# Kernel tuning notes

Hardware: AMD Instinct MI355X
Metric: run time of the kernel (lower is better)

## Reference

```python
import jax, jax.numpy as jnp
import numpy as np

B, S, F = 4, 2048, 256
H, D = 8, 32            # n_heads, width_embedding; H*D == F
LN_EPS = 1e-3           # tf.keras LayerNormalization default epsilon


def setup_inputs() -> dict:
    key = jax.random.key(0)
    ks = jax.random.split(key, 6)
    s = 1.0 / np.sqrt(F)
    return {
        "x": jax.random.normal(ks[0], (B, S, F), dtype=jnp.float32),
        "Wq": jax.random.normal(ks[1], (F, H * D), dtype=jnp.float32) * s,
        "Wk": jax.random.normal(ks[2], (F, H * D), dtype=jnp.float32) * s,
        "Wv": jax.random.normal(ks[3], (F, H * D), dtype=jnp.float32) * s,
        "Wf": jax.random.normal(ks[4], (H * D, F), dtype=jnp.float32) * s,
        "bf": jnp.zeros((F,), dtype=jnp.float32),
    }


def reference(x, Wq, Wk, Wv, Wf, bf):
    # QKV projections (no bias), split heads: [B,S,H*D] -> [B,H,S,D]
    def split(t):
        return t.reshape(B, S, H, D).transpose(0, 2, 1, 3)

    q = split(x @ Wq) / jnp.sqrt(jnp.asarray(H, x.dtype))  # NOTE: module scales by sqrt(n_heads)
    k = split(x @ Wk)
    v = split(x @ Wv)

    scores = jnp.einsum("bhsd,bhtd->bhst", q, k)          # [B,H,S,S]
    attn = jax.nn.softmax(scores, axis=-1)
    ctx = jnp.einsum("bhst,bhtd->bhsd", attn, v)           # [B,H,S,D]

    y = ctx.transpose(0, 2, 1, 3).reshape(B, S, H * D)     # merge heads
    y = jax.nn.relu(y @ Wf + bf)                            # final dense with relu

    # residual + LayerNorm(center=False, scale=False)
    z = x + y
    mean = jnp.mean(z, axis=-1, keepdims=True)
    var = jnp.var(z, axis=-1, keepdims=True)
    return (z - mean) * jax.lax.rsqrt(var + LN_EPS)
```

## Files before the change

kernel.cpp:

```cpp
#include <hip/hip_runtime.h>
#include <math.h>

#define NB 4
#define NS 2048
#define NF 256
#define NH 8
#define ND 32

constexpr float LN_EPS = 1e-3f;
constexpr float QSCALE = 0.35355339059327373f;
constexpr float LOG2E  = 1.4426950408889634f;

typedef __bf16 bf16x8 __attribute__((ext_vector_type(8)));
typedef float f32x4 __attribute__((ext_vector_type(4)));

__global__ __launch_bounds__(256)
void prep_w(const float* __restrict__ Wq, const float* __restrict__ Wk,
            const float* __restrict__ Wv, const float* __restrict__ Wf,
            unsigned short* __restrict__ wt)
{
    __shared__ float tile[64][65];
    const int wid = blockIdx.x;
    const int t = threadIdx.x;
    const int z = wid >> 4;
    const int tl = wid & 15;
    const float* W = (z == 0) ? Wq : (z == 1) ? Wk : (z == 2) ? Wv : Wf;
    const float scale = (z == 0) ? QSCALE * LOG2E : 1.0f;
    const int r0 = (tl >> 2) * 64, c0 = (tl & 3) * 64;
    const int tr = t >> 4, tc4 = (t & 15) * 4;

    #pragma unroll
    for (int p = 0; p < 4; ++p) {
        float4 v = *(const float4*)(W + (size_t)(r0 + tr + p * 16) * NF + c0 + tc4);
        tile[tr + p * 16][tc4 + 0] = v.x;
        tile[tr + p * 16][tc4 + 1] = v.y;
        tile[tr + p * 16][tc4 + 2] = v.z;
        tile[tr + p * 16][tc4 + 3] = v.w;
    }
    __syncthreads();
    #pragma unroll
    for (int p = 0; p < 4; ++p) {
        union { ushort4 u; __bf16 h[4]; } o;
        #pragma unroll
        for (int j = 0; j < 4; ++j)
            o.h[j] = (__bf16)(tile[tc4 + j][tr + p * 16] * scale);
        *(ushort4*)(wt + (size_t)z * 65536 + (size_t)(c0 + tr + p * 16) * NF + r0 + tc4) = o.u;
    }
}

__global__ __launch_bounds__(256)
void qkv_mfma(const float* __restrict__ x, const unsigned short* __restrict__ wt,
              unsigned short* __restrict__ qo, unsigned short* __restrict__ ko,
              unsigned short* __restrict__ vo)
{
    const int z = blockIdx.y;
    unsigned short* out = (z == 0) ? qo : (z == 1) ? ko : vo;
    const unsigned short* W = wt + (size_t)z * 65536;

    const int r0 = blockIdx.x * 64;
    const int t = threadIdx.x;
    const int w = t >> 6, lane = t & 63;
    const int l15 = lane & 15, lhi = lane >> 4;
    const int wr = w >> 1, wc = w & 1;

    f32x4 acc[2][8] = {};

    #pragma unroll 2
    for (int kt = 0; kt < NF; kt += 32) {
        const float* xr0 = x + (size_t)(r0 + wr * 32 + l15) * NF + kt + lhi * 8;
        const float* xr1 = x + (size_t)(r0 + wr * 32 + 16 + l15) * NF + kt + lhi * 8;
        float4 f00 = *(const float4*)xr0;
        float4 f01 = *(const float4*)(xr0 + 4);
        float4 f10 = *(const float4*)xr1;
        float4 f11 = *(const float4*)(xr1 + 4);
        bf16x8 a0, a1;
        a0[0] = (__bf16)f00.x; a0[1] = (__bf16)f00.y; a0[2] = (__bf16)f00.z; a0[3] = (__bf16)f00.w;
        a0[4] = (__bf16)f01.x; a0[5] = (__bf16)f01.y; a0[6] = (__bf16)f01.z; a0[7] = (__bf16)f01.w;
        a1[0] = (__bf16)f10.x; a1[1] = (__bf16)f10.y; a1[2] = (__bf16)f10.z; a1[3] = (__bf16)f10.w;
        a1[4] = (__bf16)f11.x; a1[5] = (__bf16)f11.y; a1[6] = (__bf16)f11.z; a1[7] = (__bf16)f11.w;
        #pragma unroll
        for (int c = 0; c < 8; ++c) {
            bf16x8 b = *(const bf16x8*)(W + (size_t)(wc * 128 + c * 16 + l15) * NF + kt + lhi * 8);
            acc[0][c] = __builtin_amdgcn_mfma_f32_16x16x32_bf16(a0, b, acc[0][c], 0, 0, 0);
            acc[1][c] = __builtin_amdgcn_mfma_f32_16x16x32_bf16(a1, b, acc[1][c], 0, 0, 0);
        }
    }

    #pragma unroll
    for (int i = 0; i < 2; ++i) {
        #pragma unroll
        for (int c = 0; c < 8; ++c) {
            const int col = wc * 128 + c * 16 + l15;
            const int h = col >> 5, d = col & 31;
            #pragma unroll
            for (int r = 0; r < 4; ++r) {
                const int row = r0 + wr * 32 + i * 16 + lhi * 4 + r;
                const int b = row >> 11, s = row & 2047;
                __bf16 o = (__bf16)acc[i][c][r];
                out[((size_t)(b * NH + h) * NS + s) * ND + d] = *(unsigned short*)&o;
            }
        }
    }
}

__global__ __launch_bounds__(256)
void attn_mfma(const unsigned short* __restrict__ q, const unsigned short* __restrict__ k,
               const unsigned short* __restrict__ v, unsigned short* __restrict__ ctxb)
{
    const int bh = blockIdx.x;
    const int s0 = blockIdx.y * 64;
    const int t = threadIdx.x;
    const int w = t >> 6;
    const int lane = t & 63;
    const int l15 = lane & 15;
    const int lhi = lane >> 4;

    __shared__ unsigned short ps[4][16][72];
    __shared__ unsigned short vt[2][32][72];

    const unsigned short* qb = q + (size_t)bh * NS * ND;
    const unsigned short* kb = k + (size_t)bh * NS * ND;
    const unsigned short* vb = v + (size_t)bh * NS * ND;

    bf16x8 qfrag = *(const bf16x8*)(qb + (size_t)(s0 + w * 16 + l15) * ND + lhi * 8);

    float lpart = 0.0f;
    f32x4 acc0 = {0.f, 0.f, 0.f, 0.f};
    f32x4 acc1 = {0.f, 0.f, 0.f, 0.f};

    const f32x4 zero = {0.f, 0.f, 0.f, 0.f};
    f32x4 sc[4];
    bf16x8 kf[4];
    {
        #pragma unroll
        for (int f = 0; f < 4; ++f) {
            bf16x8 k0 = *(const bf16x8*)(kb + (size_t)(f * 16 + l15) * ND + lhi * 8);
            sc[f] = __builtin_amdgcn_mfma_f32_16x16x32_bf16(k0, qfrag, zero, 0, 0, 0);
        }
        #pragma unroll
        for (int f = 0; f < 4; ++f)
            kf[f] = *(const bf16x8*)(kb + (size_t)(64 + f * 16 + l15) * ND + lhi * 8);
        bf16x8 vv = *(const bf16x8*)(vb + (size_t)lane * ND + w * 8);
        union { bf16x8 v8; unsigned short s[8]; } u; u.v8 = vv;
        #pragma unroll
        for (int i = 0; i < 8; ++i) vt[0][w * 8 + i][lane] = u.s[i];
    }
    __syncthreads();

    int cur = 0;
    #pragma unroll 2
    for (int tI = 0; tI < 32; ++tI) {
        const int ktn  = ((tI + 1) & 31) * 64;
        const int ktn2 = ((tI + 2) & 31) * 64;
        bf16x8 vv = *(const bf16x8*)(vb + (size_t)(ktn + lane) * ND + w * 8);
        bf16x8 kn[4];
        #pragma unroll
        for (int f = 0; f < 4; ++f)
            kn[f] = *(const bf16x8*)(kb + (size_t)(ktn2 + f * 16 + l15) * ND + lhi * 8);

        f32x4 scn[4];
        __builtin_amdgcn_s_setprio(1);
        #pragma unroll
        for (int f = 0; f < 4; ++f)
            scn[f] = __builtin_amdgcn_mfma_f32_16x16x32_bf16(kf[f], qfrag, zero, 0, 0, 0);
        __builtin_amdgcn_s_setprio(0);

        float lp[4];
        #pragma unroll
        for (int f = 0; f < 4; ++f) {
            float p0 = __builtin_amdgcn_exp2f(sc[f][0]);
            float p1 = __builtin_amdgcn_exp2f(sc[f][1]);
            float p2 = __builtin_amdgcn_exp2f(sc[f][2]);
            float p3 = __builtin_amdgcn_exp2f(sc[f][3]);
            union { ushort4 u; __bf16 h[4]; } pk;
            pk.h[0] = (__bf16)p0; pk.h[1] = (__bf16)p1;
            pk.h[2] = (__bf16)p2; pk.h[3] = (__bf16)p3;
            *(ushort4*)&ps[w][l15][f * 16 + lhi * 4] = pk.u;
            lp[f] = (p0 + p1) + (p2 + p3);
        }
        lpart += (lp[0] + lp[1]) + (lp[2] + lp[3]);

        __builtin_amdgcn_s_setprio(1);
        #pragma unroll
        for (int c = 0; c < 2; ++c) {
            bf16x8 pa  = *(const bf16x8*)&ps[w][l15][c * 32 + lhi * 8];
            bf16x8 vf0 = *(const bf16x8*)&vt[cur][l15][c * 32 + lhi * 8];
            bf16x8 vf1 = *(const bf16x8*)&vt[cur][16 + l15][c * 32 + lhi * 8];
            acc0 = __builtin_amdgcn_mfma_f32_16x16x32_bf16(pa, vf0, acc0, 0, 0, 0);
            acc1 = __builtin_amdgcn_mfma_f32_16x16x32_bf16(pa, vf1, acc1, 0, 0, 0);
        }
        __builtin_amdgcn_s_setprio(0);

        {
            union { bf16x8 v8; unsigned short s[8]; } u; u.v8 = vv;
            #pragma unroll
            for (int i = 0; i < 8; ++i) vt[cur ^ 1][w * 8 + i][lane] = u.s[i];
        }
        #pragma unroll
        for (int f = 0; f < 4; ++f) kf[f] = kn[f];
        #pragma unroll
        for (int f = 0; f < 4; ++f) sc[f] = scn[f];
        __syncthreads();
        cur ^= 1;
    }

    lpart += __shfl_xor(lpart, 16);
    lpart += __shfl_xor(lpart, 32);

    const int b = bh >> 3, h = bh & 7;
    #pragma unroll
    for (int r = 0; r < 4; ++r) {
        float li = __shfl(lpart, lhi * 4 + r);
        float inv = 1.0f / li;
        int row = s0 + w * 16 + lhi * 4 + r;
        unsigned short* op = ctxb + ((size_t)b * NS + row) * NF + h * ND;
        __bf16 o0 = (__bf16)(acc0[r] * inv);
        __bf16 o1 = (__bf16)(acc1[r] * inv);
        op[l15]      = *(unsigned short*)&o0;
        op[16 + l15] = *(unsigned short*)&o1;
    }
}

__global__ __launch_bounds__(256)
void dense_ln(const unsigned short* __restrict__ ctxb, const unsigned short* __restrict__ wft,
              const float* __restrict__ bfp, const float* __restrict__ x,
              float* __restrict__ out)
{
    const int r0 = blockIdx.x * 32;
    const int t = threadIdx.x;
    const int w = t >> 6;
    const int lane = t & 63;
    const int l15 = lane & 15;
    const int lhi = lane >> 4;

    __shared__ float zs[32][258];

    f32x4 acc[2][4] = {};

    #pragma unroll 2
    for (int kt = 0; kt < NF; kt += 32) {
        bf16x8 a0 = *(const bf16x8*)(ctxb + (size_t)(r0 + l15) * NF + kt + lhi * 8);
        bf16x8 a1 = *(const bf16x8*)(ctxb + (size_t)(r0 + 16 + l15) * NF + kt + lhi * 8);
        #pragma unroll
        for (int c = 0; c < 4; ++c) {
            bf16x8 b = *(const bf16x8*)(wft + (size_t)(w * 64 + c * 16 + l15) * NF + kt + lhi * 8);
            acc[0][c] = __builtin_amdgcn_mfma_f32_16x16x32_bf16(a0, b, acc[0][c], 0, 0, 0);
            acc[1][c] = __builtin_amdgcn_mfma_f32_16x16x32_bf16(a1, b, acc[1][c], 0, 0, 0);
        }
    }

    #pragma unroll
    for (int i = 0; i < 2; ++i) {
        #pragma unroll
        for (int c = 0; c < 4; ++c) {
            const int col = w * 64 + c * 16 + l15;
            const float bb = bfp[col];
            #pragma unroll
            for (int r = 0; r < 4; ++r) {
                const int row = i * 16 + lhi * 4 + r;
                zs[row][col] = fmaxf(acc[i][c][r] + bb, 0.0f);
            }
        }
    }
    __syncthreads();

    #pragma unroll
    for (int i = 0; i < 8; ++i) {
        const int row = w * 8 + i;
        float4 yv = *(const float4*)&zs[row][lane * 4];
        float4 xv = *(const float4*)(x + (size_t)(r0 + row) * NF + lane * 4);
        float z0 = xv.x + yv.x, z1 = xv.y + yv.y;
        float z2 = xv.z + yv.z, z3 = xv.w + yv.w;
        float sum = z0 + z1 + z2 + z3;
        float sq  = z0*z0 + z1*z1 + z2*z2 + z3*z3;
        #pragma unroll
        for (int o = 1; o < 64; o <<= 1) {
            sum += __shfl_xor(sum, o);
            sq  += __shfl_xor(sq, o);
        }
        float mean = sum * (1.0f / NF);
        float var  = sq * (1.0f / NF) - mean * mean;
        float rstd = rsqrtf(var + LN_EPS);
        float4 o4;
        o4.x = (z0 - mean) * rstd;
        o4.y = (z1 - mean) * rstd;
        o4.z = (z2 - mean) * rstd;
        o4.w = (z3 - mean) * rstd;
        *(float4*)(out + (size_t)(r0 + row) * NF + lane * 4) = o4;
    }
}

extern "C" void kernel_launch(void* const* d_in, const int* in_sizes, int n_in,
                              void* d_out, int out_size, void* d_ws, size_t ws_size,
                              hipStream_t stream)
{
    const float* x  = (const float*)d_in[0];
    const float* Wq = (const float*)d_in[1];
    const float* Wk = (const float*)d_in[2];
    const float* Wv = (const float*)d_in[3];
    const float* Wf = (const float*)d_in[4];
    const float* bf = (const float*)d_in[5];
    float* out = (float*)d_out;

    const size_t per = (size_t)NB * NH * NS * ND;
    unsigned short* q    = (unsigned short*)d_ws;
    unsigned short* kk   = q + per;
    unsigned short* vv   = kk + per;
    unsigned short* wt   = vv + per;
    unsigned short* ctxb = wt + 4 * 65536;

    prep_w<<<dim3(64), 256, 0, stream>>>(Wq, Wk, Wv, Wf, wt);
    qkv_mfma<<<dim3(128, 3), 256, 0, stream>>>(x, wt, q, kk, vv);
    attn_mfma<<<dim3(NB * NH, NS / 64), 256, 0, stream>>>(q, kk, vv, ctxb);
    dense_ln<<<dim3((NB * NS) / 32), 256, 0, stream>>>(ctxb, wt + 3 * 65536, bf, x, out);
}
```

Before: 87.81 us.

## Double attention query tile per wave, swizzle LDS, halve QKV row tile

The attention kernel now gives each wave 32 query rows instead of 16, so every K fragment and V tile loaded is reused for twice as many rows, and the grid is halved. It drops the one-iteration score pipelining, applies XOR swizzles to the P and V-transposed shared buffers to reduce bank conflicts, and the QKV projection kernel moves to 32-row tiles with twice as many blocks. The trade-off is more registers per thread and fewer attention blocks (512), which may leave the GPU underfilled and expose MFMA latency that the removed pipelining used to hide.

```diff
diff --git a/kernel.cpp b/kernel.cpp
--- a/kernel.cpp
+++ b/kernel.cpp
@@ -57,48 +57,39 @@
     unsigned short* out = (z == 0) ? qo : (z == 1) ? ko : vo;
     const unsigned short* W = wt + (size_t)z * 65536;
 
-    const int r0 = blockIdx.x * 64;
+    const int r0 = blockIdx.x * 32;
     const int t = threadIdx.x;
     const int w = t >> 6, lane = t & 63;
     const int l15 = lane & 15, lhi = lane >> 4;
     const int wr = w >> 1, wc = w & 1;
 
-    f32x4 acc[2][8] = {};
+    f32x4 acc[8] = {};
 
     #pragma unroll 2
     for (int kt = 0; kt < NF; kt += 32) {
-        const float* xr0 = x + (size_t)(r0 + wr * 32 + l15) * NF + kt + lhi * 8;
-        const float* xr1 = x + (size_t)(r0 + wr * 32 + 16 + l15) * NF + kt + lhi * 8;
-        float4 f00 = *(const float4*)xr0;
-        float4 f01 = *(const float4*)(xr0 + 4);
-        float4 f10 = *(const float4*)xr1;
-        float4 f11 = *(const float4*)(xr1 + 4);
-        bf16x8 a0, a1;
-        a0[0] = (__bf16)f00.x; a0[1] = (__bf16)f00.y; a0[2] = (__bf16)f00.z; a0[3] = (__bf16)f00.w;
-        a0[4] = (__bf16)f01.x; a0[5] = (__bf16)f01.y; a0[6] = (__bf16)f01.z; a0[7] = (__bf16)f01.w;
-        a1[0] = (__bf16)f10.x; a1[1] = (__bf16)f10.y; a1[2] = (__bf16)f10.z; a1[3] = (__bf16)f10.w;
-        a1[4] = (__bf16)f11.x; a1[5] = (__bf16)f11.y; a1[6] = (__bf16)f11.z; a1[7] = (__bf16)f11.w;
+        const float* xr = x + (size_t)(r0 + wr * 16 + l15) * NF + kt + lhi * 8;
+        float4 f0 = *(const float4*)xr;
+        float4 f1 = *(const float4*)(xr + 4);
+        bf16x8 a;
+        a[0] = (__bf16)f0.x; a[1] = (__bf16)f0.y; a[2] = (__bf16)f0.z; a[3] = (__bf16)f0.w;
+        a[4] = (__bf16)f1.x; a[5] = (__bf16)f1.y; a[6] = (__bf16)f1.z; a[7] = (__bf16)f1.w;
         #pragma unroll
         for (int c = 0; c < 8; ++c) {
             bf16x8 b = *(const bf16x8*)(W + (size_t)(wc * 128 + c * 16 + l15) * NF + kt + lhi * 8);
-            acc[0][c] = __builtin_amdgcn_mfma_f32_16x16x32_bf16(a0, b, acc[0][c], 0, 0, 0);
-            acc[1][c] = __builtin_amdgcn_mfma_f32_16x16x32_bf16(a1, b, acc[1][c], 0, 0, 0);
-        }
-    }
-
-    #pragma unroll
-    for (int i = 0; i < 2; ++i) {
-        #pragma unroll
-        for (int c = 0; c < 8; ++c) {
-            const int col = wc * 128 + c * 16 + l15;
-            const int h = col >> 5, d = col & 31;
-            #pragma unroll
-            for (int r = 0; r < 4; ++r) {
-                const int row = r0 + wr * 32 + i * 16 + lhi * 4 + r;
-                const int b = row >> 11, s = row & 2047;
-                __bf16 o = (__bf16)acc[i][c][r];
-                out[((size_t)(b * NH + h) * NS + s) * ND + d] = *(unsigned short*)&o;
-            }
+            acc[c] = __builtin_amdgcn_mfma_f32_16x16x32_bf16(a, b, acc[c], 0, 0, 0);
+        }
+    }
+
+    #pragma unroll
+    for (int c = 0; c < 8; ++c) {
+        const int col = wc * 128 + c * 16 + l15;
+        const int h = col >> 5, d = col & 31;
+        #pragma unroll
+        for (int r = 0; r < 4; ++r) {
+            const int row = r0 + wr * 16 + lhi * 4 + r;
+            const int b = row >> 11, s = row & 2047;
+            __bf16 o = (__bf16)acc[c][r];
+            out[((size_t)(b * NH + h) * NS + s) * ND + d] = *(unsigned short*)&o;
         }
     }
 }
@@ -108,116 +99,138 @@
                const unsigned short* __restrict__ v, unsigned short* __restrict__ ctxb)
 {
     const int bh = blockIdx.x;
-    const int s0 = blockIdx.y * 64;
+    const int s0 = blockIdx.y * 128;
     const int t = threadIdx.x;
     const int w = t >> 6;
     const int lane = t & 63;
     const int l15 = lane & 15;
     const int lhi = lane >> 4;
-
-    __shared__ unsigned short ps[4][16][72];
+    const int sx  = l15 & 8;
+    const int wsx = (w & 1) * 8;
+
+    __shared__ unsigned short ps[4][32][72];
     __shared__ unsigned short vt[2][32][72];
 
     const unsigned short* qb = q + (size_t)bh * NS * ND;
     const unsigned short* kb = k + (size_t)bh * NS * ND;
     const unsigned short* vb = v + (size_t)bh * NS * ND;
 
-    bf16x8 qfrag = *(const bf16x8*)(qb + (size_t)(s0 + w * 16 + l15) * ND + lhi * 8);
-
-    float lpart = 0.0f;
-    f32x4 acc0 = {0.f, 0.f, 0.f, 0.f};
-    f32x4 acc1 = {0.f, 0.f, 0.f, 0.f};
-
-    const f32x4 zero = {0.f, 0.f, 0.f, 0.f};
-    f32x4 sc[4];
+    bf16x8 qf0 = *(const bf16x8*)(qb + (size_t)(s0 + w * 32 + l15) * ND + lhi * 8);
+    bf16x8 qf1 = *(const bf16x8*)(qb + (size_t)(s0 + w * 32 + 16 + l15) * ND + lhi * 8);
+
+    float lp0 = 0.f, lp1 = 0.f;
+    f32x4 acc00 = {0.f,0.f,0.f,0.f}, acc01 = {0.f,0.f,0.f,0.f};
+    f32x4 acc10 = {0.f,0.f,0.f,0.f}, acc11 = {0.f,0.f,0.f,0.f};
+
     bf16x8 kf[4];
+    #pragma unroll
+    for (int f = 0; f < 4; ++f)
+        kf[f] = *(const bf16x8*)(kb + (size_t)(f * 16 + l15) * ND + lhi * 8);
     {
-        #pragma unroll
-        for (int f = 0; f < 4; ++f) {
-            bf16x8 k0 = *(const bf16x8*)(kb + (size_t)(f * 16 + l15) * ND + lhi * 8);
-            sc[f] = __builtin_amdgcn_mfma_f32_16x16x32_bf16(k0, qfrag, zero, 0, 0, 0);
-        }
-        #pragma unroll
-        for (int f = 0; f < 4; ++f)
-            kf[f] = *(const bf16x8*)(kb + (size_t)(64 + f * 16 + l15) * ND + lhi * 8);
         bf16x8 vv = *(const bf16x8*)(vb + (size_t)lane * ND + w * 8);
         union { bf16x8 v8; unsigned short s[8]; } u; u.v8 = vv;
         #pragma unroll
-        for (int i = 0; i < 8; ++i) vt[0][w * 8 + i][lane] = u.s[i];
+        for (int i = 0; i < 8; ++i) vt[0][w * 8 + i][lane ^ wsx] = u.s[i];
     }
     __syncthreads();
 
     int cur = 0;
     #pragma unroll 2
     for (int tI = 0; tI < 32; ++tI) {
-        const int ktn  = ((tI + 1) & 31) * 64;
-        const int ktn2 = ((tI + 2) & 31) * 64;
+        const int ktn = ((tI + 1) & 31) * 64;
         bf16x8 vv = *(const bf16x8*)(vb + (size_t)(ktn + lane) * ND + w * 8);
         bf16x8 kn[4];
         #pragma unroll
         for (int f = 0; f < 4; ++f)
-            kn[f] = *(const bf16x8*)(kb + (size_t)(ktn2 + f * 16 + l15) * ND + lhi * 8);
-
-        f32x4 scn[4];
+            kn[f] = *(const bf16x8*)(kb + (size_t)(ktn + f * 16 + l15) * ND + lhi * 8);
+
+        const f32x4 zero = {0.f, 0.f, 0.f, 0.f};
+        f32x4 sc0[4], sc1[4];
         __builtin_amdgcn_s_setprio(1);
         #pragma unroll
-        for (int f = 0; f < 4; ++f)
-            scn[f] = __builtin_amdgcn_mfma_f32_16x16x32_bf16(kf[f], qfrag, zero, 0, 0, 0);
+        for (int f = 0; f < 4; ++f) {
+            sc0[f] = __builtin_amdgcn_mfma_f32_16x16x32_bf16(kf[f], qf0, zero, 0, 0, 0);
+            sc1[f] = __builtin_amdgcn_mfma_f32_16x16x32_bf16(kf[f], qf1, zero, 0, 0, 0);
+        }
         __builtin_amdgcn_s_setprio(0);
 
-        float lp[4];
+        float a0 = 0.f, a1 = 0.f;
         #pragma unroll
         for (int f = 0; f < 4; ++f) {
-            float p0 = __builtin_amdgcn_exp2f(sc[f][0]);
-            float p1 = __builtin_amdgcn_exp2f(sc[f][1]);
-            float p2 = __builtin_amdgcn_exp2f(sc[f][2]);
-            float p3 = __builtin_amdgcn_exp2f(sc[f][3]);
+            float p0 = __builtin_amdgcn_exp2f(sc0[f][0]);
+            float p1 = __builtin_amdgcn_exp2f(sc0[f][1]);
+            float p2 = __builtin_amdgcn_exp2f(sc0[f][2]);
+            float p3 = __builtin_amdgcn_exp2f(sc0[f][3]);
             union { ushort4 u; __bf16 h[4]; } pk;
             pk.h[0] = (__bf16)p0; pk.h[1] = (__bf16)p1;
             pk.h[2] = (__bf16)p2; pk.h[3] = (__bf16)p3;
-            *(ushort4*)&ps[w][l15][f * 16 + lhi * 4] = pk.u;
-            lp[f] = (p0 + p1) + (p2 + p3);
-        }
-        lpart += (lp[0] + lp[1]) + (lp[2] + lp[3]);
+            *(ushort4*)&ps[w][l15][(f * 16 + lhi * 4) ^ sx] = pk.u;
+            a0 += (p0 + p1) + (p2 + p3);
+        }
+        #pragma unroll
+        for (int f = 0; f < 4; ++f) {
+            float p0 = __builtin_amdgcn_exp2f(sc1[f][0]);
+            float p1 = __builtin_amdgcn_exp2f(sc1[f][1]);
+            float p2 = __builtin_amdgcn_exp2f(sc1[f][2]);
+            float p3 = __builtin_amdgcn_exp2f(sc1[f][3]);
+            union { ushort4 u; __bf16 h[4]; } pk;
+            pk.h[0] = (__bf16)p0; pk.h[1] = (__bf16)p1;
+            pk.h[2] = (__bf16)p2; pk.h[3] = (__bf16)p3;
+            *(ushort4*)&ps[w][16 + l15][(f * 16 + lhi * 4) ^ sx] = pk.u;
+            a1 += (p0 + p1) + (p2 + p3);
+        }
+        lp0 += a0; lp1 += a1;
 
         __builtin_amdgcn_s_setprio(1);
         #pragma unroll
         for (int c = 0; c < 2; ++c) {
-            bf16x8 pa  = *(const bf16x8*)&ps[w][l15][c * 32 + lhi * 8];
-            bf16x8 vf0 = *(const bf16x8*)&vt[cur][l15][c * 32 + lhi * 8];
-            bf16x8 vf1 = *(const bf16x8*)&vt[cur][16 + l15][c * 32 + lhi * 8];
-            acc0 = __builtin_amdgcn_mfma_f32_16x16x32_bf16(pa, vf0, acc0, 0, 0, 0);
-            acc1 = __builtin_amdgcn_mfma_f32_16x16x32_bf16(pa, vf1, acc1, 0, 0, 0);
+            const int co = (c * 32 + lhi * 8) ^ sx;
+            bf16x8 pa0 = *(const bf16x8*)&ps[w][l15][co];
+            bf16x8 pa1 = *(const bf16x8*)&ps[w][16 + l15][co];
+            bf16x8 vf0 = *(const bf16x8*)&vt[cur][l15][co];
+            bf16x8 vf1 = *(const bf16x8*)&vt[cur][16 + l15][co];
+            acc00 = __builtin_amdgcn_mfma_f32_16x16x32_bf16(pa0, vf0, acc00, 0, 0, 0);
+            acc01 = __builtin_amdgcn_mfma_f32_16x16x32_bf16(pa0, vf1, acc01, 0, 0, 0);
+            acc10 = __builtin_amdgcn_mfma_f32_16x16x32_bf16(pa1, vf0, acc10, 0, 0, 0);
+            acc11 = __builtin_amdgcn_mfma_f32_16x16x32_bf16(pa1, vf1, acc11, 0, 0, 0);
         }
         __builtin_amdgcn_s_setprio(0);
 
         {
             union { bf16x8 v8; unsigned short s[8]; } u; u.v8 = vv;
             #pragma unroll
-            for (int i = 0; i < 8; ++i) vt[cur ^ 1][w * 8 + i][lane] = u.s[i];
+            for (int i = 0; i < 8; ++i) vt[cur ^ 1][w * 8 + i][lane ^ wsx] = u.s[i];
         }
         #pragma unroll
         for (int f = 0; f < 4; ++f) kf[f] = kn[f];
-        #pragma unroll
-        for (int f = 0; f < 4; ++f) sc[f] = scn[f];
         __syncthreads();
         cur ^= 1;
     }
 
-    lpart += __shfl_xor(lpart, 16);
-    lpart += __shfl_xor(lpart, 32);
+    lp0 += __shfl_xor(lp0, 16);
+    lp0 += __shfl_xor(lp0, 32);
+    lp1 += __shfl_xor(lp1, 16);
+    lp1 += __shfl_xor(lp1, 32);
 
     const int b = bh >> 3, h = bh & 7;
     #pragma unroll
     for (int r = 0; r < 4; ++r) {
-        float li = __shfl(lpart, lhi * 4 + r);
-        float inv = 1.0f / li;
-        int row = s0 + w * 16 + lhi * 4 + r;
-        unsigned short* op = ctxb + ((size_t)b * NS + row) * NF + h * ND;
-        __bf16 o0 = (__bf16)(acc0[r] * inv);
-        __bf16 o1 = (__bf16)(acc1[r] * inv);
-        op[l15]      = *(unsigned short*)&o0;
-        op[16 + l15] = *(unsigned short*)&o1;
+        float li0 = __shfl(lp0, lhi * 4 + r);
+        float li1 = __shfl(lp1, lhi * 4 + r);
+        float inv0 = 1.0f / li0;
+        float inv1 = 1.0f / li1;
+        int row0 = s0 + w * 32 + lhi * 4 + r;
+        int row1 = row0 + 16;
+        unsigned short* op0 = ctxb + ((size_t)b * NS + row0) * NF + h * ND;
+        unsigned short* op1 = ctxb + ((size_t)b * NS + row1) * NF + h * ND;
+        __bf16 o00 = (__bf16)(acc00[r] * inv0);
+        __bf16 o01 = (__bf16)(acc01[r] * inv0);
+        __bf16 o10 = (__bf16)(acc10[r] * inv1);
+        __bf16 o11 = (__bf16)(acc11[r] * inv1);
+        op0[l15]      = *(unsigned short*)&o00;
+        op0[16 + l15] = *(unsigned short*)&o01;
+        op1[l15]      = *(unsigned short*)&o10;
+        op1[16 + l15] = *(unsigned short*)&o11;
     }
 }
 
@@ -310,7 +323,7 @@
     unsigned short* ctxb = wt + 4 * 65536;
 
     prep_w<<<dim3(64), 256, 0, stream>>>(Wq, Wk, Wv, Wf, wt);
-    qkv_mfma<<<dim3(128, 3), 256, 0, stream>>>(x, wt, q, kk, vv);
-    attn_mfma<<<dim3(NB * NH, NS / 64), 256, 0, stream>>>(q, kk, vv, ctxb);
+    qkv_mfma<<<dim3(256, 3), 256, 0, stream>>>(x, wt, q, kk, vv);
+    attn_mfma<<<dim3(NB * NH, NS / 128), 256, 0, stream>>>(q, kk, vv, ctxb);
     dense_ln<<<dim3((NB * NS) / 32), 256, 0, stream>>>(ctxb, wt + 3 * 65536, bf, x, out);
 }
```

Result: no change. 87.14 us (-0.8%).
